# Optimization experiments

Measured on AMD Instinct MI355X. Metric: run time of the kernel, lower is better.

The kernel has to match this reference:

```python
import jax, jax.numpy as jnp
import numpy as np

HEADS = 4
DIM_HEAD = 32


def setup_inputs() -> dict:
    key = jax.random.key(0)
    k0, k1, k2, k3 = jax.random.split(key, 4)
    b, C, H, W = 32, 128, 64, 64
    hidden = HEADS * DIM_HEAD
    x = jax.random.normal(k0, (b, C, H, W), dtype=jnp.float32)
    g = jnp.ones((C,), dtype=jnp.float32)                      # RMSNorm gain
    w_qkv = jax.random.normal(k1, (3 * hidden, C), dtype=jnp.float32) * 0.05
    mem_kv = jax.random.normal(k2, (2, HEADS, DIM_HEAD, 4), dtype=jnp.float32)
    w_out = jax.random.normal(k3, (C, hidden), dtype=jnp.float32) * 0.05
    b_out = jnp.zeros((C,), dtype=jnp.float32)
    return {"x": x, "g": g, "w_qkv": w_qkv, "mem_kv": mem_kv,
            "w_out": w_out, "b_out": b_out}


def reference(x, g, w_qkv, mem_kv, w_out, b_out):
    b, C, H, W = x.shape
    heads = mem_kv.shape[1]
    dh = mem_kv.shape[2]
    hidden = heads * dh
    scale = dh ** -0.5

    # RMSNorm variant: F.normalize along channel dim * g * sqrt(C)
    norm = jnp.maximum(jnp.sqrt(jnp.sum(x * x, axis=1, keepdims=True)), 1e-12)
    xn = x / norm * g[None, :, None, None] * (C ** 0.5)

    # 1x1 conv qkv projection (no bias)
    qkv = jnp.einsum('bchw,oc->bohw', xn, w_qkv)  # [b, 3*hidden, H, W]
    q, k, v = jnp.split(qkv, 3, axis=1)
    n = H * W
    q = q.reshape(b, heads, dh, n)
    k = k.reshape(b, heads, dh, n)
    v = v.reshape(b, heads, dh, n)

    # prepend memory kv slots along the token dim
    mk = jnp.broadcast_to(mem_kv[0][None], (b, heads, dh, mem_kv.shape[3]))
    mv = jnp.broadcast_to(mem_kv[1][None], (b, heads, dh, mem_kv.shape[3]))
    k = jnp.concatenate([mk, k], axis=-1)
    v = jnp.concatenate([mv, v], axis=-1)

    q = jax.nn.softmax(q, axis=-2) * scale   # softmax over feature dim d
    k = jax.nn.softmax(k, axis=-1)           # softmax over token dim n

    context = jnp.einsum('bhdn,bhen->bhde', k, v)   # [b,h,d,e]
    out = jnp.einsum('bhde,bhdn->bhen', context, q)  # [b,h,e,n]
    out = out.reshape(b, hidden, H, W)

    # 1x1 conv output projection (with bias)
    return jnp.einsum('bchw,oc->bohw', out, w_out) + b_out[None, :, None, None]
```

## Files before the change

kernel.cpp:

```cpp
#include <hip/hip_runtime.h>
#include <hip/hip_bf16.h>

typedef __attribute__((ext_vector_type(8))) short short8;
typedef __attribute__((ext_vector_type(4))) float f32x4;


__device__ __forceinline__ unsigned short f2bf(float f) {
  unsigned u = __float_as_uint(f);
  u += 0x7fff + ((u >> 16) & 1);
  return (unsigned short)(u >> 16);
}
__device__ __forceinline__ float bf2f(unsigned short s) {
  return __uint_as_float(((unsigned)s) << 16);
}

__global__ void k0_init(const float* __restrict__ wqkv, const float* __restrict__ g,
                        float* __restrict__ ws) {
  int tid = blockIdx.x * blockDim.x + threadIdx.x;
  int stride = gridDim.x * blockDim.x;
  unsigned short* Wf = (unsigned short*)(ws + 2424832);
  for (int i = tid; i < 49152; i += stride) {
    int o = i >> 7, c = i & 127;
    int f = (o >> 4) * 4 + (c >> 5);
    int lane = (o & 15) + (((c >> 3) & 3) << 4);
    Wf[f * 512 + lane * 8 + (c & 7)] = f2bf(wqkv[o * 128 + c]);
  }
  float* gs = ws + 2449408;
  if (tid < 128) gs[tid] = g[tid] * 11.313708498984761f;
}

__global__ __launch_bounds__(256, 4) void k1_qkv(
    const float* __restrict__ x, const unsigned short* __restrict__ Wf,
    const float* __restrict__ gs, unsigned short* __restrict__ Sp,
    unsigned short* __restrict__ Zp, unsigned short* __restrict__ qbf) {
  __shared__ __align__(16) unsigned short xnf[16 * 512];
  __shared__ unsigned short kbuf[128 * 66];
  __shared__ unsigned short vbuf[128 * 66];
  __shared__ float ssred[256];
  const int b = blockIdx.x >> 5, grp = blockIdx.x & 31;
  const int tid = threadIdx.x;
  const int p = tid & 63, w = tid >> 6;
  const int chunk = __builtin_amdgcn_readfirstlane(w);
  const int l = p, quad = l >> 4, l16 = l & 15;

  const int h4 = chunk, d0 = l16, eq = quad;
  float sacc0[8] = {}, sacc1[8] = {};
  float z0 = 0.f, z1 = 0.f;

  for (int t = 0; t < 2; t++) {
    const int tile = grp * 2 + t;
    const int P = tile * 64 + p;
    const float* xb = x + (size_t)b * 524288 + P;
    float xr[32];
    float ss = 0.f;
#pragma unroll
    for (int i = 0; i < 32; i++) {
      float v = xb[(size_t)(w * 32 + i) * 4096];
      xr[i] = v; ss += v * v;
    }
    ssred[w * 64 + p] = ss;
    __syncthreads();
    float tot = ssred[p] + ssred[64 + p] + ssred[128 + p] + ssred[192 + p];
    float inv = 1.0f / fmaxf(sqrtf(tot), 1e-12f);
#pragma unroll
    for (int q8 = 0; q8 < 4; q8++) {
      short8 v8;
#pragma unroll
      for (int j = 0; j < 8; j++) {
        int i = q8 * 8 + j;
        v8[j] = (short)f2bf(xr[i] * gs[w * 32 + i] * inv);
      }
      *(short8*)&xnf[(w * 4 + (p >> 4)) * 512 + ((p & 15) + q8 * 16) * 8] = v8;
    }
    __syncthreads();

    const short8* Wfv = (const short8*)Wf;
#pragma unroll
    for (int s = 0; s < 3; s++) {
      f32x4 acc[2][4] = {};
#pragma unroll
      for (int k0 = 0; k0 < 4; k0++) {
        short8 bfr[4];
#pragma unroll
        for (int n0 = 0; n0 < 4; n0++)
          bfr[n0] = *(const short8*)&xnf[(k0 * 4 + n0) * 512 + l * 8];
#pragma unroll
        for (int off = 0; off < 2; off++) {
          short8 afr = Wfv[((chunk * 6 + 2 * s + off) * 4 + k0) * 64 + l];
#pragma unroll
          for (int n0 = 0; n0 < 4; n0++)
            acc[off][n0] = __builtin_amdgcn_mfma_f32_16x16x32_bf16(afr, bfr[n0], acc[off][n0], 0, 0, 0);
        }
      }
      const int o0 = chunk * 96 + 32 * s;
      if (o0 < 128) {
        int h = o0 >> 5;
#pragma unroll
        for (int n0 = 0; n0 < 4; n0++) {
          float m = -1e30f;
#pragma unroll
          for (int off = 0; off < 2; off++)
#pragma unroll
            for (int r = 0; r < 4; r++) m = fmaxf(m, acc[off][n0][r]);
          m = fmaxf(m, __shfl_xor(m, 16, 64));
          m = fmaxf(m, __shfl_xor(m, 32, 64));
          float e[2][4]; float sum = 0.f;
#pragma unroll
          for (int off = 0; off < 2; off++)
#pragma unroll
            for (int r = 0; r < 4; r++) {
              e[off][r] = __expf(acc[off][n0][r] - m);
              sum += e[off][r];
            }
          sum += __shfl_xor(sum, 16, 64);
          sum += __shfl_xor(sum, 32, 64);
          float rs = 0.17677669529663687f / sum;
          int qbase = ((b * 64 + tile) * 16 + h * 4 + n0) * 512;
#pragma unroll
          for (int off = 0; off < 2; off++)
#pragma unroll
            for (int r = 0; r < 4; r++) {
              int lane2 = l16 + ((off * 2 + (quad >> 1)) << 4);
              int jj = (quad & 1) * 4 + r;
              qbf[qbase + lane2 * 8 + jj] = f2bf(e[off][r] * rs);
            }
        }
      } else if (o0 < 256) {
        int h = (o0 - 128) >> 5;
#pragma unroll
        for (int n0 = 0; n0 < 4; n0++)
#pragma unroll
          for (int off = 0; off < 2; off++)
#pragma unroll
            for (int r = 0; r < 4; r++) {
              int row = h * 32 + off * 16 + quad * 4 + r;
              kbuf[row * 66 + n0 * 16 + l16] = f2bf(__expf(acc[off][n0][r]));
            }
      } else {
        int h = (o0 - 256) >> 5;
#pragma unroll
        for (int n0 = 0; n0 < 4; n0++)
#pragma unroll
          for (int off = 0; off < 2; off++)
#pragma unroll
            for (int r = 0; r < 4; r++) {
              int row = h * 32 + off * 16 + quad * 4 + r;
              vbuf[row * 66 + n0 * 16 + l16] = f2bf(acc[off][n0][r]);
            }
      }
    }
    __syncthreads();

    const unsigned short* kr0 = kbuf + (h4 * 32 + d0) * 66;
    const unsigned short* kr1 = kr0 + 16 * 66;
    const unsigned short* vr = vbuf + (h4 * 32 + 8 * eq) * 66;
#pragma unroll 4
    for (int pp = 0; pp < 32; pp++) {
      unsigned ka = *(const unsigned*)&kr0[2 * pp];
      unsigned kc = *(const unsigned*)&kr1[2 * pp];
      float k0e = __uint_as_float(ka << 16), k0o = __uint_as_float(ka & 0xffff0000u);
      float k1e = __uint_as_float(kc << 16), k1o = __uint_as_float(kc & 0xffff0000u);
      z0 += k0e + k0o; z1 += k1e + k1o;
#pragma unroll
      for (int j = 0; j < 8; j++) {
        unsigned vv = *(const unsigned*)&vr[j * 66 + 2 * pp];
        float ve = __uint_as_float(vv << 16), vo = __uint_as_float(vv & 0xffff0000u);
        sacc0[j] += k0e * ve + k0o * vo;
        sacc1[j] += k1e * ve + k1o * vo;
      }
    }
  }

  unsigned short* Spb = Sp + (size_t)(b * 32 + grp) * 4096;
  short8 s0, s1;
#pragma unroll
  for (int j = 0; j < 8; j++) { s0[j] = (short)f2bf(sacc0[j]); s1[j] = (short)f2bf(sacc1[j]); }
  *(short8*)&Spb[(h4 * 32 + d0) * 32 + 8 * eq] = s0;
  *(short8*)&Spb[(h4 * 32 + d0 + 16) * 32 + 8 * eq] = s1;
  if (eq == 0) {
    Zp[(b * 32 + grp) * 128 + h4 * 32 + d0] = f2bf(z0);
    Zp[(b * 32 + grp) * 128 + h4 * 32 + d0 + 16] = f2bf(z1);
  }
}

__global__ void k2_ctx(const unsigned short* __restrict__ Sp, const unsigned short* __restrict__ Zp,
                       const float* __restrict__ memkv, const float* __restrict__ wout,
                       unsigned short* __restrict__ Mtf) {
  __shared__ float C[1024];
  __shared__ float zinv[128];
  const int b = blockIdx.x >> 2, qr = blockIdx.x & 3, tid = threadIdx.x;
  if (tid < 128) {
    float z = 0.f;
#pragma unroll
    for (int g = 0; g < 32; g++) z += bf2f(Zp[(b * 32 + g) * 128 + tid]);
    float zm = 0.f;
#pragma unroll
    for (int j = 0; j < 4; j++) zm += __expf(memkv[tid * 4 + j]);
    zinv[tid] = 1.0f / (z + zm);
  }
  __syncthreads();
  for (int i = tid; i < 1024; i += 256) {
    int idx = qr * 1024 + i;
    int hd = idx >> 5, e = idx & 31, h = hd >> 5;
    float s = 0.f;
#pragma unroll
    for (int g = 0; g < 32; g++) s += bf2f(Sp[(size_t)(b * 32 + g) * 4096 + idx]);
    float sm = 0.f;
#pragma unroll
    for (int j = 0; j < 4; j++)
      sm += __expf(memkv[hd * 4 + j]) * memkv[512 + (h * 32 + e) * 4 + j];
    C[i] = (s + sm) * zinv[hd];
  }
  __syncthreads();
  for (int i = tid; i < 4096; i += 256) {
    int hd = qr * 32 + (i >> 7);
    int o = i & 127, h = hd >> 5;
    float a = 0.f;
#pragma unroll
    for (int e = 0; e < 32; e++) a += wout[o * 128 + h * 32 + e] * C[(i >> 7) * 32 + e];
    int f = (o >> 4) * 4 + (hd >> 5);
    int lane = (o & 15) + (((hd >> 3) & 3) << 4);
    Mtf[(size_t)b * 16384 + f * 512 + lane * 8 + (hd & 7)] = f2bf(a);
  }
}

__global__ __launch_bounds__(256) void k3_out(
    const unsigned short* __restrict__ qbf, const unsigned short* __restrict__ Mtf,
    const float* __restrict__ bout, float* __restrict__ out) {
  __shared__ __align__(16) unsigned short qf[16 * 512];
  __shared__ __align__(16) float obuf[128 * 68];
  const int b = blockIdx.x >> 6, tile = blockIdx.x & 63;
  const int tid = threadIdx.x;
  const int l = tid & 63, quad = l >> 4, l16 = l & 15;
  const int chunk = __builtin_amdgcn_readfirstlane(tid >> 6);
  const short8* qv = (const short8*)qbf;
  const int base = ((b * 64 + tile) * 16) * 64;
#pragma unroll
  for (int r = 0; r < 4; r++) {
    int cid = tid + 256 * r;
    *(short8*)&qf[cid * 8] = qv[base + cid];
  }
  __syncthreads();
  f32x4 acc[2][4] = {};
  const short8* Mv = (const short8*)Mtf;
#pragma unroll
  for (int k0 = 0; k0 < 4; k0++) {
    short8 bfr[4];
#pragma unroll
    for (int n0 = 0; n0 < 4; n0++)
      bfr[n0] = *(const short8*)&qf[(k0 * 4 + n0) * 512 + l * 8];
#pragma unroll
    for (int mm = 0; mm < 2; mm++) {
      short8 afr = Mv[((size_t)b * 32 + (chunk * 2 + mm) * 4 + k0) * 64 + l];
#pragma unroll
      for (int n0 = 0; n0 < 4; n0++)
        acc[mm][n0] = __builtin_amdgcn_mfma_f32_16x16x32_bf16(afr, bfr[n0], acc[mm][n0], 0, 0, 0);
    }
  }
#pragma unroll
  for (int mm = 0; mm < 2; mm++)
#pragma unroll
    for (int r = 0; r < 4; r++) {
      float bv = bout[chunk * 32 + mm * 16 + quad * 4 + r];
#pragma unroll
      for (int n0 = 0; n0 < 4; n0++) {
        int o = chunk * 32 + mm * 16 + quad * 4 + r;
        obuf[o * 68 + n0 * 16 + l16] = acc[mm][n0][r] + bv;
      }
    }
  __syncthreads();
#pragma unroll
  for (int rr = 0; rr < 8; rr++) {
    int idx = tid + 256 * rr;
    int row = idx >> 4, c4 = idx & 15;
    f32x4 v = *(const f32x4*)&obuf[row * 68 + c4 * 4];
    *(f32x4*)&out[((size_t)b * 128 + row) * 4096 + tile * 64 + c4 * 4] = v;
  }
}

extern "C" void kernel_launch(void* const* d_in, const int* in_sizes, int n_in,
                              void* d_out, int out_size, void* d_ws, size_t ws_size,
                              hipStream_t stream) {
  const float* x     = (const float*)d_in[0];
  const float* g     = (const float*)d_in[1];
  const float* wqkv  = (const float*)d_in[2];
  const float* memkv = (const float*)d_in[3];
  const float* wout  = (const float*)d_in[4];
  const float* bout  = (const float*)d_in[5];
  float* out = (float*)d_out;
  float* ws = (float*)d_ws;
  unsigned short* Sp  = (unsigned short*)ws;
  unsigned short* Zp  = (unsigned short*)(ws + 2097152);
  unsigned short* Mtf = (unsigned short*)(ws + 2162688);
  unsigned short* Wf  = (unsigned short*)(ws + 2424832);
  float* gs  = ws + 2449408;
  unsigned short* qbf = (unsigned short*)(ws + 2449536);

  k0_init<<<128, 256, 0, stream>>>(wqkv, g, ws);
  k1_qkv<<<1024, 256, 0, stream>>>(x, Wf, gs, Sp, Zp, qbf);
  k2_ctx<<<128, 256, 0, stream>>>(Sp, Zp, memkv, wout, Mtf);
  k3_out<<<2048, 256, 0, stream>>>(qbf, Mtf, bout, out);
}
```

Before: 195.6 us.

## Compute k^T v context and k-sum with MFMA, swizzled LDS, fewer blocks

Replaces the scalar FMA loop that accumulated the per-head k·v context and k row sums with bf16 MFMA instructions, using a ones vector to get the sums. The k/v LDS buffers move from padded rows to an XOR-swizzled layout so the MFMA fragment loads avoid bank conflicts. Each block now covers four tiles instead of two with half as many blocks, which halves the partial-sum traffic read by k2 (whose indexing is updated to the fragment layout). The wave-to-output mapping is remapped, B fragments are hoisted into registers, q stores are vectorised, and launch bounds are relaxed to allow more registers at the cost of occupancy.

```diff
diff --git a/kernel.cpp b/kernel.cpp
--- a/kernel.cpp
+++ b/kernel.cpp
@@ -2,6 +2,7 @@
 #include <hip/hip_bf16.h>
 
 typedef __attribute__((ext_vector_type(8))) short short8;
+typedef __attribute__((ext_vector_type(4))) short bf16x4;
 typedef __attribute__((ext_vector_type(4))) float f32x4;
 
 
@@ -29,33 +30,36 @@
   if (tid < 128) gs[tid] = g[tid] * 11.313708498984761f;
 }
 
-__global__ __launch_bounds__(256, 4) void k1_qkv(
+__global__ __launch_bounds__(256, 2) void k1_qkv(
     const float* __restrict__ x, const unsigned short* __restrict__ Wf,
     const float* __restrict__ gs, unsigned short* __restrict__ Sp,
     unsigned short* __restrict__ Zp, unsigned short* __restrict__ qbf) {
   __shared__ __align__(16) unsigned short xnf[16 * 512];
-  __shared__ unsigned short kbuf[128 * 66];
-  __shared__ unsigned short vbuf[128 * 66];
+  __shared__ __align__(16) unsigned short kbuf[128 * 64];
+  __shared__ __align__(16) unsigned short vbuf[128 * 64];
   __shared__ float ssred[256];
-  const int b = blockIdx.x >> 5, grp = blockIdx.x & 31;
+  const int b = blockIdx.x >> 4, grp = blockIdx.x & 15;
   const int tid = threadIdx.x;
   const int p = tid & 63, w = tid >> 6;
   const int chunk = __builtin_amdgcn_readfirstlane(w);
   const int l = p, quad = l >> 4, l16 = l & 15;
 
-  const int h4 = chunk, d0 = l16, eq = quad;
-  float sacc0[8] = {}, sacc1[8] = {};
-  float z0 = 0.f, z1 = 0.f;
-
-  for (int t = 0; t < 2; t++) {
-    const int tile = grp * 2 + t;
+  short8 ones;
+#pragma unroll
+  for (int j = 0; j < 8; j++) ones[j] = (short)0x3F80;
+
+  f32x4 accS[2][2] = {};
+  f32x4 accZ[2] = {};
+
+  for (int t = 0; t < 4; t++) {
+    const int tile = grp * 4 + t;
     const int P = tile * 64 + p;
     const float* xb = x + (size_t)b * 524288 + P;
     float xr[32];
     float ss = 0.f;
 #pragma unroll
     for (int i = 0; i < 32; i++) {
-      float v = xb[(size_t)(w * 32 + i) * 4096];
+      float v = xb[(size_t)(chunk * 32 + i) * 4096];
       xr[i] = v; ss += v * v;
     }
     ssred[w * 64 + p] = ss;
@@ -68,11 +72,15 @@
 #pragma unroll
       for (int j = 0; j < 8; j++) {
         int i = q8 * 8 + j;
-        v8[j] = (short)f2bf(xr[i] * gs[w * 32 + i] * inv);
-      }
-      *(short8*)&xnf[(w * 4 + (p >> 4)) * 512 + ((p & 15) + q8 * 16) * 8] = v8;
+        v8[j] = (short)f2bf(xr[i] * gs[chunk * 32 + i] * inv);
+      }
+      *(short8*)&xnf[(chunk * 4 + (p >> 4)) * 512 + ((p & 15) + q8 * 16) * 8] = v8;
     }
     __syncthreads();
+
+    short8 bfr[16];
+#pragma unroll
+    for (int i = 0; i < 16; i++) bfr[i] = *(const short8*)&xnf[i * 512 + l * 8];
 
     const short8* Wfv = (const short8*)Wf;
 #pragma unroll
@@ -80,21 +88,15 @@
       f32x4 acc[2][4] = {};
 #pragma unroll
       for (int k0 = 0; k0 < 4; k0++) {
-        short8 bfr[4];
-#pragma unroll
-        for (int n0 = 0; n0 < 4; n0++)
-          bfr[n0] = *(const short8*)&xnf[(k0 * 4 + n0) * 512 + l * 8];
 #pragma unroll
         for (int off = 0; off < 2; off++) {
-          short8 afr = Wfv[((chunk * 6 + 2 * s + off) * 4 + k0) * 64 + l];
+          short8 afr = Wfv[((s * 8 + chunk * 2 + off) * 4 + k0) * 64 + l];
 #pragma unroll
           for (int n0 = 0; n0 < 4; n0++)
-            acc[off][n0] = __builtin_amdgcn_mfma_f32_16x16x32_bf16(afr, bfr[n0], acc[off][n0], 0, 0, 0);
+            acc[off][n0] = __builtin_amdgcn_mfma_f32_16x16x32_bf16(afr, bfr[k0 * 4 + n0], acc[off][n0], 0, 0, 0);
         }
       }
-      const int o0 = chunk * 96 + 32 * s;
-      if (o0 < 128) {
-        int h = o0 >> 5;
+      if (s == 0) {
 #pragma unroll
         for (int n0 = 0; n0 < 4; n0++) {
           float m = -1e30f;
@@ -115,71 +117,80 @@
           sum += __shfl_xor(sum, 16, 64);
           sum += __shfl_xor(sum, 32, 64);
           float rs = 0.17677669529663687f / sum;
-          int qbase = ((b * 64 + tile) * 16 + h * 4 + n0) * 512;
-#pragma unroll
-          for (int off = 0; off < 2; off++)
+          int qbase = ((b * 64 + tile) * 16 + chunk * 4 + n0) * 512;
+#pragma unroll
+          for (int off = 0; off < 2; off++) {
+            int lane2 = l16 + ((off * 2 + (quad >> 1)) << 4);
+            bf16x4 qv;
+#pragma unroll
+            for (int r = 0; r < 4; r++) qv[r] = (short)f2bf(e[off][r] * rs);
+            *(bf16x4*)&qbf[qbase + lane2 * 8 + (quad & 1) * 4] = qv;
+          }
+        }
+      } else if (s == 1) {
+#pragma unroll
+        for (int off = 0; off < 2; off++)
+#pragma unroll
+          for (int n0 = 0; n0 < 4; n0++)
 #pragma unroll
             for (int r = 0; r < 4; r++) {
-              int lane2 = l16 + ((off * 2 + (quad >> 1)) << 4);
-              int jj = (quad & 1) * 4 + r;
-              qbf[qbase + lane2 * 8 + jj] = f2bf(e[off][r] * rs);
-            }
-        }
-      } else if (o0 < 256) {
-        int h = (o0 - 128) >> 5;
-#pragma unroll
-        for (int n0 = 0; n0 < 4; n0++)
-#pragma unroll
-          for (int off = 0; off < 2; off++)
-#pragma unroll
-            for (int r = 0; r < 4; r++) {
-              int row = h * 32 + off * 16 + quad * 4 + r;
-              kbuf[row * 66 + n0 * 16 + l16] = f2bf(__expf(acc[off][n0][r]));
+              int row = off * 16 + quad * 4 + r;
+              int px = n0 * 16 + l16;
+              kbuf[(chunk * 32 + row) * 64 + (px ^ ((row & 7) << 3))] = f2bf(__expf(acc[off][n0][r]));
             }
       } else {
-        int h = (o0 - 256) >> 5;
-#pragma unroll
-        for (int n0 = 0; n0 < 4; n0++)
-#pragma unroll
-          for (int off = 0; off < 2; off++)
+#pragma unroll
+        for (int off = 0; off < 2; off++)
+#pragma unroll
+          for (int n0 = 0; n0 < 4; n0++)
 #pragma unroll
             for (int r = 0; r < 4; r++) {
-              int row = h * 32 + off * 16 + quad * 4 + r;
-              vbuf[row * 66 + n0 * 16 + l16] = f2bf(acc[off][n0][r]);
+              int row = off * 16 + quad * 4 + r;
+              int px = n0 * 16 + l16;
+              vbuf[(chunk * 32 + row) * 64 + (px ^ ((row & 7) << 3))] = f2bf(acc[off][n0][r]);
             }
       }
     }
-    __syncthreads();
-
-    const unsigned short* kr0 = kbuf + (h4 * 32 + d0) * 66;
-    const unsigned short* kr1 = kr0 + 16 * 66;
-    const unsigned short* vr = vbuf + (h4 * 32 + 8 * eq) * 66;
-#pragma unroll 4
-    for (int pp = 0; pp < 32; pp++) {
-      unsigned ka = *(const unsigned*)&kr0[2 * pp];
-      unsigned kc = *(const unsigned*)&kr1[2 * pp];
-      float k0e = __uint_as_float(ka << 16), k0o = __uint_as_float(ka & 0xffff0000u);
-      float k1e = __uint_as_float(kc << 16), k1o = __uint_as_float(kc & 0xffff0000u);
-      z0 += k0e + k0o; z1 += k1e + k1o;
-#pragma unroll
-      for (int j = 0; j < 8; j++) {
-        unsigned vv = *(const unsigned*)&vr[j * 66 + 2 * pp];
-        float ve = __uint_as_float(vv << 16), vo = __uint_as_float(vv & 0xffff0000u);
-        sacc0[j] += k0e * ve + k0o * vo;
-        sacc1[j] += k1e * ve + k1o * vo;
-      }
-    }
-  }
-
-  unsigned short* Spb = Sp + (size_t)(b * 32 + grp) * 4096;
-  short8 s0, s1;
-#pragma unroll
-  for (int j = 0; j < 8; j++) { s0[j] = (short)f2bf(sacc0[j]); s1[j] = (short)f2bf(sacc1[j]); }
-  *(short8*)&Spb[(h4 * 32 + d0) * 32 + 8 * eq] = s0;
-  *(short8*)&Spb[(h4 * 32 + d0 + 16) * 32 + 8 * eq] = s1;
-  if (eq == 0) {
-    Zp[(b * 32 + grp) * 128 + h4 * 32 + d0] = f2bf(z0);
-    Zp[(b * 32 + grp) * 128 + h4 * 32 + d0 + 16] = f2bf(z1);
+
+    const unsigned short* kb = kbuf + chunk * 2048;
+    const unsigned short* vb = vbuf + chunk * 2048;
+#pragma unroll
+    for (int kk = 0; kk < 2; kk++) {
+      int cofs = (kk * 32 + quad * 8) ^ ((l16 & 7) << 3);
+      short8 ak[2], av[2];
+#pragma unroll
+      for (int mm = 0; mm < 2; mm++) {
+        ak[mm] = *(const short8*)&kb[(mm * 16 + l16) * 64 + cofs];
+        av[mm] = *(const short8*)&vb[(mm * 16 + l16) * 64 + cofs];
+      }
+#pragma unroll
+      for (int mm = 0; mm < 2; mm++) {
+#pragma unroll
+        for (int nn = 0; nn < 2; nn++)
+          accS[mm][nn] = __builtin_amdgcn_mfma_f32_16x16x32_bf16(ak[mm], av[nn], accS[mm][nn], 0, 0, 0);
+        accZ[mm] = __builtin_amdgcn_mfma_f32_16x16x32_bf16(ak[mm], ones, accZ[mm], 0, 0, 0);
+      }
+    }
+  }
+
+  unsigned short* Spb = Sp + (size_t)(b * 16 + grp) * 4096 + chunk * 1024;
+#pragma unroll
+  for (int mm = 0; mm < 2; mm++)
+#pragma unroll
+    for (int nn = 0; nn < 2; nn++) {
+      bf16x4 sv;
+#pragma unroll
+      for (int r = 0; r < 4; r++) sv[r] = (short)f2bf(accS[mm][nn][r]);
+      *(bf16x4*)&Spb[(mm * 2 + nn) * 256 + l * 4] = sv;
+    }
+  if (l16 == 0) {
+#pragma unroll
+    for (int mm = 0; mm < 2; mm++) {
+      bf16x4 zv;
+#pragma unroll
+      for (int r = 0; r < 4; r++) zv[r] = (short)f2bf(accZ[mm][r]);
+      *(bf16x4*)&Zp[(b * 16 + grp) * 128 + chunk * 32 + mm * 16 + quad * 4] = zv;
+    }
   }
 }
 
@@ -192,7 +203,7 @@
   if (tid < 128) {
     float z = 0.f;
 #pragma unroll
-    for (int g = 0; g < 32; g++) z += bf2f(Zp[(b * 32 + g) * 128 + tid]);
+    for (int g = 0; g < 16; g++) z += bf2f(Zp[(b * 16 + g) * 128 + tid]);
     float zm = 0.f;
 #pragma unroll
     for (int j = 0; j < 4; j++) zm += __expf(memkv[tid * 4 + j]);
@@ -201,10 +212,11 @@
   __syncthreads();
   for (int i = tid; i < 1024; i += 256) {
     int idx = qr * 1024 + i;
-    int hd = idx >> 5, e = idx & 31, h = hd >> 5;
+    int hd = idx >> 5, e = idx & 31, h = hd >> 5, d = hd & 31;
+    int fofs = h * 1024 + ((d >> 4) * 2 + (e >> 4)) * 256 + ((e & 15) + ((d >> 2) & 3) * 16) * 4 + (d & 3);
     float s = 0.f;
 #pragma unroll
-    for (int g = 0; g < 32; g++) s += bf2f(Sp[(size_t)(b * 32 + g) * 4096 + idx]);
+    for (int g = 0; g < 16; g++) s += bf2f(Sp[(size_t)(b * 16 + g) * 4096 + fofs]);
     float sm = 0.f;
 #pragma unroll
     for (int j = 0; j < 4; j++)
@@ -297,7 +309,7 @@
   unsigned short* qbf = (unsigned short*)(ws + 2449536);
 
   k0_init<<<128, 256, 0, stream>>>(wqkv, g, ws);
-  k1_qkv<<<1024, 256, 0, stream>>>(x, Wf, gs, Sp, Zp, qbf);
+  k1_qkv<<<512, 256, 0, stream>>>(x, Wf, gs, Sp, Zp, qbf);
   k2_ctx<<<128, 256, 0, stream>>>(Sp, Zp, memkv, wout, Mtf);
   k3_out<<<2048, 256, 0, stream>>>(qbf, Mtf, bout, out);
 }
```

Measured after the change: 228.7 us. +16.9%, slower.
